# Kernel tuning notes

Measured on AMD Instinct MI355X. Metric: run time of the kernel, lower is better.

## Reference

```python
import jax, jax.numpy as jnp
import numpy as np


def setup_inputs() -> dict:
    key = jax.random.key(0)
    k1, k2, k3 = jax.random.split(key, 3)
    B, C, H, W = 16, 256, 128, 128
    r = 16  # channels // reduction
    x = jax.random.normal(k1, (B, C, H, W), dtype=jnp.float32)
    # 1x1 conv kernels flattened to linear weights (fan-in scaled init)
    w1 = jax.random.normal(k2, (r, C), dtype=jnp.float32) * (1.0 / np.sqrt(C))
    b1 = jnp.zeros((r,), dtype=jnp.float32)
    w2 = jax.random.normal(k3, (C, r), dtype=jnp.float32) * (1.0 / np.sqrt(r))
    b2 = jnp.zeros((C,), dtype=jnp.float32)
    return {"x": x, "w1": w1, "b1": b1, "w2": w2, "b2": b2}


def reference(x, w1, b1, w2, b2):
    b, c, h, w = x.shape
    n = h * w
    x_flat = x.reshape(b, c, n)
    mu = x_flat.mean(axis=2, keepdims=True)
    xc = x_flat - mu  # [b, c, n]
    # v[b,i] = mean_j cov[b,i,j] where cov = xc @ xc^T / (n-1).
    # Algebraic reassociation: mean_j sum_k xc[i,k] xc[j,k] = sum_k xc[i,k] * s[k] / c
    # with s[k] = sum_j xc[j,k]. Avoids the O(C^2 * n) bmm; same math.
    s = xc.sum(axis=1)  # [b, n]
    denom = jnp.float32(max(1, n - 1) * c)
    v = jnp.einsum('bcn,bn->bc', xc, s) / denom  # [b, c]
    # MLP of 1x1 convs on a [b,c,1,1] descriptor == two linear layers
    h1 = jax.nn.relu(v @ w1.T + b1)              # [b, r]
    gate = jax.nn.sigmoid(h1 @ w2.T + b2)        # [b, c]
    return x * gate[:, :, None, None]
```

## Files before the change

### kernel.cpp

```cpp
#include <hip/hip_runtime.h>

#define B_ 16
#define C_ 256
#define N_ 16384
#define R_ 16
#define SUB_ 32
#define LSTR_ 257

typedef float f32x4 __attribute__((ext_vector_type(4)));

template<int NSUB>
__global__ __launch_bounds__(256, 4)
void kA(const float* __restrict__ x,
        float* __restrict__ Ppart,
        float* __restrict__ RSpart,
        int blocksPerBatch) {
    const int blk = blockIdx.x;
    const int b = blockIdx.y;
    const int t = threadIdx.x;

    __shared__ float tile[SUB_][LSTR_];
    __shared__ float csum_part[8][32];
    __shared__ float colsum[SUB_];

    const int nbase = blk * (NSUB * SUB_);
    const int kq = t & 7;
    const int crow = t >> 3;

    float accP = 0.f, accRS = 0.f;

    for (int s = 0; s < NSUB; ++s) {
        const int n0 = nbase + s * SUB_;
#pragma unroll
        for (int r = 0; r < 8; ++r) {
            const int c = crow + (r << 5);
            float4 v = *reinterpret_cast<const float4*>(
                x + ((size_t)b * C_ + c) * N_ + n0 + (kq << 2));
            tile[(kq << 2) + 0][c] = v.x;
            tile[(kq << 2) + 1][c] = v.y;
            tile[(kq << 2) + 2][c] = v.z;
            tile[(kq << 2) + 3][c] = v.w;
        }
        __syncthreads();
        {
            const int n = t & 31, oct = t >> 5;
            float cs = 0.f;
#pragma unroll
            for (int i = 0; i < 32; ++i) cs += tile[n][(oct << 5) + i];
            csum_part[oct][n] = cs;
        }
        __syncthreads();
        if (t < SUB_) {
            float cs = 0.f;
#pragma unroll
            for (int o = 0; o < 8; ++o) cs += csum_part[o][t];
            colsum[t] = cs;
        }
        __syncthreads();
#pragma unroll
        for (int n = 0; n < SUB_; ++n) {
            const float tv = tile[n][t];
            accP += tv * colsum[n];
            accRS += tv;
        }
        __syncthreads();
    }
    Ppart [((size_t)b * blocksPerBatch + blk) * C_ + t] = accP;
    RSpart[((size_t)b * blocksPerBatch + blk) * C_ + t] = accRS;
}

__global__ void kB(const float* __restrict__ Ppart,
                   const float* __restrict__ RSpart,
                   const float* __restrict__ w1, const float* __restrict__ b1,
                   const float* __restrict__ w2, const float* __restrict__ b2,
                   float* __restrict__ gate, int blocksPerBatch) {
    const int b = blockIdx.x;
    const int t = threadIdx.x;

    float P = 0.f, RS = 0.f;
    for (int k = 0; k < blocksPerBatch; ++k) {
        P  += Ppart [((size_t)b * blocksPerBatch + k) * C_ + t];
        RS += RSpart[((size_t)b * blocksPerBatch + k) * C_ + t];
    }

    __shared__ float red[4];
    float s = RS;
#pragma unroll
    for (int off = 32; off; off >>= 1) s += __shfl_down(s, off, 64);
    if ((t & 63) == 0) red[t >> 6] = s;
    __syncthreads();
    const float T = red[0] + red[1] + red[2] + red[3];
    const float M = T / (float)N_;
    const float denom = (float)(N_ - 1) * (float)C_;

    __shared__ float vl[C_];
    vl[t] = (P - M * RS) / denom;
    __syncthreads();

    __shared__ float hpart[R_][16];
    __shared__ float h1[R_];
    {
        const int i = t >> 4, cc = t & 15;
        float a = 0.f;
#pragma unroll
        for (int k = 0; k < 16; ++k)
            a += vl[(cc << 4) + k] * w1[i * C_ + (cc << 4) + k];
        hpart[i][cc] = a;
    }
    __syncthreads();
    if (t < R_) {
        float a = b1[t];
#pragma unroll
        for (int k = 0; k < 16; ++k) a += hpart[t][k];
        h1[t] = a > 0.f ? a : 0.f;
    }
    __syncthreads();

    float a = b2[t];
#pragma unroll
    for (int i = 0; i < R_; ++i) a += h1[i] * w2[t * R_ + i];
    gate[b * C_ + t] = 1.f / (1.f + __expf(-a));
}

__global__ void kC(const float* __restrict__ x,
                   const float* __restrict__ gate,
                   float* __restrict__ out) {
    const size_t total4 = (size_t)B_ * C_ * N_ / 4;
    for (size_t i = (size_t)blockIdx.x * blockDim.x + threadIdx.x; i < total4;
         i += (size_t)gridDim.x * blockDim.x) {
        const int bc = (int)(i >> 12);
        const float g = gate[bc];
        float4 vx = reinterpret_cast<const float4*>(x)[i];
        f32x4 r;
        r.x = vx.x * g; r.y = vx.y * g; r.z = vx.z * g; r.w = vx.w * g;
        __builtin_nontemporal_store(r, reinterpret_cast<f32x4*>(out) + i);
    }
}

extern "C" void kernel_launch(void* const* d_in, const int* in_sizes, int n_in,
                              void* d_out, int out_size, void* d_ws, size_t ws_size,
                              hipStream_t stream) {
    (void)in_sizes; (void)n_in; (void)out_size;
    const float* x  = (const float*)d_in[0];
    const float* w1 = (const float*)d_in[1];
    const float* b1 = (const float*)d_in[2];
    const float* w2 = (const float*)d_in[3];
    const float* b2 = (const float*)d_in[4];
    float* out = (float*)d_out;

    const size_t need64 = (size_t)(2 * B_ * 64 * C_ + B_ * C_) * sizeof(float);
    const int bpb = (ws_size >= need64) ? 64 : 32;

    float* ws     = (float*)d_ws;
    float* Ppart  = ws;
    float* RSpart = Ppart + (size_t)B_ * bpb * C_;
    float* gate   = RSpart + (size_t)B_ * bpb * C_;

    if (bpb == 64) {
        hipLaunchKernelGGL((kA<8>), dim3(64, B_), dim3(256), 0, stream,
                           x, Ppart, RSpart, 64);
    } else {
        hipLaunchKernelGGL((kA<16>), dim3(32, B_), dim3(256), 0, stream,
                           x, Ppart, RSpart, 32);
    }
    hipLaunchKernelGGL(kB, dim3(B_), dim3(256), 0, stream,
                       Ppart, RSpart, w1, b1, w2, b2, gate, bpb);
    hipLaunchKernelGGL(kC, dim3(2048), dim3(256), 0, stream,
                       x, gate, out);
}
```

Measured before the change: 156.6 us.

## Double-buffer global loads in the stats kernel and transpose the LDS tile layout

The reduction kernel now prefetches the next 32-column slab of x into a second register buffer while the current slab is staged in LDS and reduced. This overlaps global-load latency with the LDS work. The LDS tile is changed to a channel-major [256][33] layout with float4 stores and reads, and the __syncthreads calls become explicit lgkmcnt waits plus raw s_barrier. The occupancy hint in launch_bounds is dropped and the workspace-size fallback is removed. The float4 LDS accesses on an odd row stride risk misaligned access, and the extra register buffer may lower occupancy.

```diff
diff --git a/kernel.cpp b/kernel.cpp
--- a/kernel.cpp
+++ b/kernel.cpp
@@ -5,12 +5,15 @@
 #define N_ 16384
 #define R_ 16
 #define SUB_ 32
-#define LSTR_ 257
 
 typedef float f32x4 __attribute__((ext_vector_type(4)));
 
+__device__ __forceinline__ float4 ldf4(const float* p) {
+    return *reinterpret_cast<const float4*>(p);
+}
+
 template<int NSUB>
-__global__ __launch_bounds__(256, 4)
+__global__ __launch_bounds__(256)
 void kA(const float* __restrict__ x,
         float* __restrict__ Ppart,
         float* __restrict__ RSpart,
@@ -18,55 +21,73 @@
     const int blk = blockIdx.x;
     const int b = blockIdx.y;
     const int t = threadIdx.x;
-
-    __shared__ float tile[SUB_][LSTR_];
-    __shared__ float csum_part[8][32];
-    __shared__ float colsum[SUB_];
-
-    const int nbase = blk * (NSUB * SUB_);
     const int kq = t & 7;
     const int crow = t >> 3;
 
+    __shared__ float tile[C_][33];
+    __shared__ float csp[8][32];
+    __shared__ float colsum[SUB_];
+
+    const float* xb = x + (size_t)b * C_ * N_
+                    + (size_t)blk * (NSUB * SUB_) + (kq << 2);
+
+    float4 pA[8], pB[8];
     float accP = 0.f, accRS = 0.f;
 
-    for (int s = 0; s < NSUB; ++s) {
-        const int n0 = nbase + s * SUB_;
 #pragma unroll
-        for (int r = 0; r < 8; ++r) {
-            const int c = crow + (r << 5);
-            float4 v = *reinterpret_cast<const float4*>(
-                x + ((size_t)b * C_ + c) * N_ + n0 + (kq << 2));
-            tile[(kq << 2) + 0][c] = v.x;
-            tile[(kq << 2) + 1][c] = v.y;
-            tile[(kq << 2) + 2][c] = v.z;
-            tile[(kq << 2) + 3][c] = v.w;
-        }
-        __syncthreads();
-        {
-            const int n = t & 31, oct = t >> 5;
-            float cs = 0.f;
-#pragma unroll
-            for (int i = 0; i < 32; ++i) cs += tile[n][(oct << 5) + i];
-            csum_part[oct][n] = cs;
-        }
-        __syncthreads();
-        if (t < SUB_) {
-            float cs = 0.f;
-#pragma unroll
-            for (int o = 0; o < 8; ++o) cs += csum_part[o][t];
-            colsum[t] = cs;
-        }
-        __syncthreads();
-#pragma unroll
-        for (int n = 0; n < SUB_; ++n) {
-            const float tv = tile[n][t];
-            accP += tv * colsum[n];
-            accRS += tv;
-        }
-        __syncthreads();
+    for (int r = 0; r < 8; ++r)
+        pA[r] = ldf4(xb + (size_t)(crow + (r << 5)) * N_);
+
+#define PHASE(CUR, NXT, S)                                                     \
+    {                                                                          \
+               \
+        if ((S) + 1 < NSUB) {                                                  \
+            _Pragma("unroll")                                                  \
+            for (int r = 0; r < 8; ++r)                                        \
+                NXT[r] = ldf4(xb + (size_t)(crow + (r << 5)) * N_              \
+                              + ((S) + 1) * SUB_);                             \
+        }                                                                      \
+        _Pragma("unroll")                                                      \
+        for (int r = 0; r < 8; ++r)                                            \
+            *reinterpret_cast<float4*>(&tile[crow + (r << 5)][kq << 2]) = CUR[r]; \
+        asm volatile("s_waitcnt lgkmcnt(0)" ::: "memory");                     \
+        __builtin_amdgcn_s_barrier();                                          \
+        {     \
+            const int n = t & 31, oct = t >> 5;                                \
+            float cs = 0.f;                                                    \
+            _Pragma("unroll")                                                  \
+            for (int i = 0; i < 32; ++i) cs += tile[(oct << 5) + i][n];        \
+            csp[oct][n] = cs;                                                  \
+        }                                                                      \
+        asm volatile("s_waitcnt lgkmcnt(0)" ::: "memory");                     \
+        __builtin_amdgcn_s_barrier();                                          \
+        if (t < SUB_) {                                                        \
+            float cs = 0.f;                                                    \
+            _Pragma("unroll")                                                  \
+            for (int o = 0; o < 8; ++o) cs += csp[o][t];                       \
+            colsum[t] = cs;                                                    \
+        }                                                                      \
+        asm volatile("s_waitcnt lgkmcnt(0)" ::: "memory");                     \
+        __builtin_amdgcn_s_barrier();                                          \
+        _Pragma("unroll")                                                      \
+        for (int j = 0; j < 8; ++j) {           \
+            float4 xv = *reinterpret_cast<float4*>(&tile[t][j << 2]);          \
+            float4 cl = *reinterpret_cast<float4*>(&colsum[j << 2]);           \
+            accP += xv.x * cl.x + xv.y * cl.y + xv.z * cl.z + xv.w * cl.w;     \
+            accRS += xv.x + xv.y + xv.z + xv.w;                                \
+        }                                                                      \
+        __builtin_amdgcn_s_barrier();   \
     }
-    Ppart [((size_t)b * blocksPerBatch + blk) * C_ + t] = accP;
-    RSpart[((size_t)b * blocksPerBatch + blk) * C_ + t] = accRS;
+
+    for (int s = 0; s < NSUB; s += 2) {
+        PHASE(pA, pB, s)
+        PHASE(pB, pA, s + 1)
+    }
+#undef PHASE
+
+    const size_t base = ((size_t)b * blocksPerBatch + blk) * C_;
+    Ppart [base + t] = accP;
+    RSpart[base + t] = accRS;
 }
 
 __global__ void kB(const float* __restrict__ Ppart,
@@ -140,7 +161,7 @@
 extern "C" void kernel_launch(void* const* d_in, const int* in_sizes, int n_in,
                               void* d_out, int out_size, void* d_ws, size_t ws_size,
                               hipStream_t stream) {
-    (void)in_sizes; (void)n_in; (void)out_size;
+    (void)in_sizes; (void)n_in; (void)out_size; (void)ws_size;
     const float* x  = (const float*)d_in[0];
     const float* w1 = (const float*)d_in[1];
     const float* b1 = (const float*)d_in[2];
@@ -148,21 +169,15 @@
     const float* b2 = (const float*)d_in[4];
     float* out = (float*)d_out;
 
-    const size_t need64 = (size_t)(2 * B_ * 64 * C_ + B_ * C_) * sizeof(float);
-    const int bpb = (ws_size >= need64) ? 64 : 32;
+    const int bpb = 64;
 
     float* ws     = (float*)d_ws;
     float* Ppart  = ws;
     float* RSpart = Ppart + (size_t)B_ * bpb * C_;
     float* gate   = RSpart + (size_t)B_ * bpb * C_;
 
-    if (bpb == 64) {
-        hipLaunchKernelGGL((kA<8>), dim3(64, B_), dim3(256), 0, stream,
-                           x, Ppart, RSpart, 64);
-    } else {
-        hipLaunchKernelGGL((kA<16>), dim3(32, B_), dim3(256), 0, stream,
-                           x, Ppart, RSpart, 32);
-    }
+    hipLaunchKernelGGL((kA<8>), dim3(bpb, B_), dim3(256), 0, stream,
+                       x, Ppart, RSpart, bpb);
     hipLaunchKernelGGL(kB, dim3(B_), dim3(256), 0, stream,
                        Ppart, RSpart, w1, b1, w2, b2, gate, bpb);
     hipLaunchKernelGGL(kC, dim3(2048), dim3(256), 0, stream,
```

New measurement: 157.8 us. No clear change (+0.7%).

## Split covariance reduction into column-sum pass and per-channel dot-product pass

Applied to the files above, without the earlier changes.

Replaces the single tiled LDS-transpose reduction kernel with two passes: one kernel sums x over channels per spatial position into a workspace, and a second kernel computes per-channel dot products against those column sums along with row sums, reducing to v per channel. This removes shared-memory transposes and multiple barriers per tile. In exchange, x is read an extra time from memory, and an intermediate column-sum buffer is written and read.

```diff
diff --git a/kernel.cpp b/kernel.cpp
--- a/kernel.cpp
+++ b/kernel.cpp
@@ -4,97 +4,82 @@
 #define C_ 256
 #define N_ 16384
 #define R_ 16
-#define SUB_ 32
-#define LSTR_ 257
 
 typedef float f32x4 __attribute__((ext_vector_type(4)));
 
-template<int NSUB>
-__global__ __launch_bounds__(256, 4)
-void kA(const float* __restrict__ x,
-        float* __restrict__ Ppart,
-        float* __restrict__ RSpart,
-        int blocksPerBatch) {
-    const int blk = blockIdx.x;
+__device__ __forceinline__ float4 ldf4(const float* p) {
+    return *reinterpret_cast<const float4*>(p);
+}
+
+__global__ void k1_colsum(const float* __restrict__ x,
+                          float* __restrict__ part) {
+    const int b = blockIdx.x;
+    const int tile = blockIdx.y;
+    const int half = blockIdx.z;
+    const int n0 = tile * 1024 + threadIdx.x * 4;
+    const float* xb = x + ((size_t)b * C_ + half * 128) * N_ + n0;
+
+    float4 acc = make_float4(0.f, 0.f, 0.f, 0.f);
+#pragma unroll 8
+    for (int c = 0; c < 128; ++c) {
+        float4 v = ldf4(xb + (size_t)c * N_);
+        acc.x += v.x; acc.y += v.y; acc.z += v.z; acc.w += v.w;
+    }
+    *reinterpret_cast<float4*>(part + (size_t)(b * 2 + half) * N_ + n0) = acc;
+}
+
+__global__ void k2_v(const float* __restrict__ x,
+                     const float* __restrict__ part,
+                     float* __restrict__ v) {
+    const int c = blockIdx.x;
     const int b = blockIdx.y;
     const int t = threadIdx.x;
 
-    __shared__ float tile[SUB_][LSTR_];
-    __shared__ float csum_part[8][32];
-    __shared__ float colsum[SUB_];
+    const float* xr = x + ((size_t)b * C_ + c) * N_;
+    const float* p0 = part + (size_t)(b * 2 + 0) * N_;
+    const float* p1 = part + (size_t)(b * 2 + 1) * N_;
 
-    const int nbase = blk * (NSUB * SUB_);
-    const int kq = t & 7;
-    const int crow = t >> 3;
+    float P = 0.f, RS = 0.f, Tacc = 0.f;
+#pragma unroll 4
+    for (int n = t * 4; n < N_; n += 1024) {
+        float4 xv = ldf4(xr + n);
+        float4 a = ldf4(p0 + n);
+        float4 bb = ldf4(p1 + n);
+        float4 cs = make_float4(a.x + bb.x, a.y + bb.y, a.z + bb.z, a.w + bb.w);
+        P += xv.x * cs.x + xv.y * cs.y + xv.z * cs.z + xv.w * cs.w;
+        RS += xv.x + xv.y + xv.z + xv.w;
+        Tacc += cs.x + cs.y + cs.z + cs.w;
+    }
 
-    float accP = 0.f, accRS = 0.f;
-
-    for (int s = 0; s < NSUB; ++s) {
-        const int n0 = nbase + s * SUB_;
 #pragma unroll
-        for (int r = 0; r < 8; ++r) {
-            const int c = crow + (r << 5);
-            float4 v = *reinterpret_cast<const float4*>(
-                x + ((size_t)b * C_ + c) * N_ + n0 + (kq << 2));
-            tile[(kq << 2) + 0][c] = v.x;
-            tile[(kq << 2) + 1][c] = v.y;
-            tile[(kq << 2) + 2][c] = v.z;
-            tile[(kq << 2) + 3][c] = v.w;
-        }
-        __syncthreads();
-        {
-            const int n = t & 31, oct = t >> 5;
-            float cs = 0.f;
-#pragma unroll
-            for (int i = 0; i < 32; ++i) cs += tile[n][(oct << 5) + i];
-            csum_part[oct][n] = cs;
-        }
-        __syncthreads();
-        if (t < SUB_) {
-            float cs = 0.f;
-#pragma unroll
-            for (int o = 0; o < 8; ++o) cs += csum_part[o][t];
-            colsum[t] = cs;
-        }
-        __syncthreads();
-#pragma unroll
-        for (int n = 0; n < SUB_; ++n) {
-            const float tv = tile[n][t];
-            accP += tv * colsum[n];
-            accRS += tv;
-        }
-        __syncthreads();
+    for (int off = 32; off; off >>= 1) {
+        P    += __shfl_down(P, off, 64);
+        RS   += __shfl_down(RS, off, 64);
+        Tacc += __shfl_down(Tacc, off, 64);
     }
-    Ppart [((size_t)b * blocksPerBatch + blk) * C_ + t] = accP;
-    RSpart[((size_t)b * blocksPerBatch + blk) * C_ + t] = accRS;
+    __shared__ float redP[4], redR[4], redT[4];
+    if ((t & 63) == 0) {
+        redP[t >> 6] = P; redR[t >> 6] = RS; redT[t >> 6] = Tacc;
+    }
+    __syncthreads();
+    if (t == 0) {
+        const float Pf = redP[0] + redP[1] + redP[2] + redP[3];
+        const float RSf = redR[0] + redR[1] + redR[2] + redR[3];
+        const float Tf = redT[0] + redT[1] + redT[2] + redT[3];
+        const float denom = (float)(N_ - 1) * (float)C_;
+        v[b * C_ + c] = (Pf - (Tf / (float)N_) * RSf) / denom;
+    }
 }
 
-__global__ void kB(const float* __restrict__ Ppart,
-                   const float* __restrict__ RSpart,
+__global__ void kB(const float* __restrict__ v,
                    const float* __restrict__ w1, const float* __restrict__ b1,
                    const float* __restrict__ w2, const float* __restrict__ b2,
-                   float* __restrict__ gate, int blocksPerBatch) {
+                   float* __restrict__ gate) {
     const int b = blockIdx.x;
     const int t = threadIdx.x;
 
-    float P = 0.f, RS = 0.f;
-    for (int k = 0; k < blocksPerBatch; ++k) {
-        P  += Ppart [((size_t)b * blocksPerBatch + k) * C_ + t];
-        RS += RSpart[((size_t)b * blocksPerBatch + k) * C_ + t];
-    }
-
-    __shared__ float red[4];
-    float s = RS;
-#pragma unroll
-    for (int off = 32; off; off >>= 1) s += __shfl_down(s, off, 64);
-    if ((t & 63) == 0) red[t >> 6] = s;
-    __syncthreads();
-    const float T = red[0] + red[1] + red[2] + red[3];
-    const float M = T / (float)N_;
-    const float denom = (float)(N_ - 1) * (float)C_;
-
     __shared__ float vl[C_];
-    vl[t] = (P - M * RS) / denom;
+    vl[t] = v[b * C_ + t];
     __syncthreads();
 
     __shared__ float hpart[R_][16];
@@ -140,7 +125,7 @@
 extern "C" void kernel_launch(void* const* d_in, const int* in_sizes, int n_in,
                               void* d_out, int out_size, void* d_ws, size_t ws_size,
                               hipStream_t stream) {
-    (void)in_sizes; (void)n_in; (void)out_size;
+    (void)in_sizes; (void)n_in; (void)out_size; (void)ws_size;
     const float* x  = (const float*)d_in[0];
     const float* w1 = (const float*)d_in[1];
     const float* b1 = (const float*)d_in[2];
@@ -148,23 +133,17 @@
     const float* b2 = (const float*)d_in[4];
     float* out = (float*)d_out;
 
-    const size_t need64 = (size_t)(2 * B_ * 64 * C_ + B_ * C_) * sizeof(float);
-    const int bpb = (ws_size >= need64) ? 64 : 32;
+    float* ws   = (float*)d_ws;
+    float* part = ws;
+    float* v    = part + (size_t)2 * B_ * N_;
+    float* gate = v + B_ * C_;
 
-    float* ws     = (float*)d_ws;
-    float* Ppart  = ws;
-    float* RSpart = Ppart + (size_t)B_ * bpb * C_;
-    float* gate   = RSpart + (size_t)B_ * bpb * C_;
-
-    if (bpb == 64) {
-        hipLaunchKernelGGL((kA<8>), dim3(64, B_), dim3(256), 0, stream,
-                           x, Ppart, RSpart, 64);
-    } else {
-        hipLaunchKernelGGL((kA<16>), dim3(32, B_), dim3(256), 0, stream,
-                           x, Ppart, RSpart, 32);
-    }
+    hipLaunchKernelGGL(k1_colsum, dim3(B_, 16, 2), dim3(256), 0, stream,
+                       x, part);
+    hipLaunchKernelGGL(k2_v, dim3(C_, B_), dim3(256), 0, stream,
+                       x, part, v);
     hipLaunchKernelGGL(kB, dim3(B_), dim3(256), 0, stream,
-                       Ppart, RSpart, w1, b1, w2, b2, gate, bpb);
+                       v, w1, b1, w2, b2, gate);
     hipLaunchKernelGGL(kC, dim3(2048), dim3(256), 0, stream,
                        x, gate, out);
 }
```

Result: slower. 170.3 us (+8.7%).
